# Kernel optimization log

Hardware: AMD Instinct MI355X
Metric: run time of the kernel (lower is better)

Reference implementation:

```python
import jax, jax.numpy as jnp
import numpy as np
from jax import lax


def conv2d(x, w, padding):
    # x: [B,C,H,W], w: [O,I,kh,kw]; torch Conv2d == cross-correlation, same as lax default
    return lax.conv_general_dilated(x, w, (1, 1), padding,
                                    dimension_numbers=('NCHW', 'OIHW', 'NCHW'))


def setup_inputs() -> dict:
    key = jax.random.key(0)
    ks = jax.random.split(key, 16)
    B, C1, C2, H1, W1, H2, W2, ratio = 8, 256, 512, 64, 64, 32, 32, 8
    Cr = C1 // ratio  # 32
    s = 0.05
    return {
        'x1': jax.random.normal(ks[0], (B, C1, H1, W1), jnp.float32),
        'x2': jax.random.normal(ks[1], (B, C2, H2, W2), jnp.float32),
        'wq': jax.random.normal(ks[2], (Cr, C1, 3, 3), jnp.float32) * s,
        'wk': jax.random.normal(ks[3], (Cr, C2, 3, 3), jnp.float32) * s,
        'wv': jax.random.normal(ks[4], (C1, C2, 3, 3), jnp.float32) * s,
        'wc': jax.random.normal(ks[5], (1, C1, 1, 1), jnp.float32) * s,
        'wch': jax.random.normal(ks[6], (C1, C1, 3, 3), jnp.float32) * s,
        'wt1': jax.random.normal(ks[7], (Cr, C1, 1, 1), jnp.float32) * s,
        'bt1': jax.random.normal(ks[8], (Cr,), jnp.float32) * s,
        'ln_g': jnp.ones((Cr, 1, 1), jnp.float32),
        'ln_b': jnp.zeros((Cr, 1, 1), jnp.float32),
        'wt2': jax.random.normal(ks[9], (C1, Cr, 1, 1), jnp.float32) * s,
        'bt2': jax.random.normal(ks[10], (C1,), jnp.float32) * s,
    }


def reference(x1, x2, wq, wk, wv, wc, wch, wt1, bt1, ln_g, ln_b, wt2, bt2):
    B, C1, H1, W1 = x1.shape
    N1 = H1 * W1
    N2 = x2.shape[2] * x2.shape[3]
    eps = 1e-5

    # spatial cross-attention branch
    q = conv2d(x1, wq, 'SAME').reshape(B, -1, N1)          # [B,Cr,N1]
    k = conv2d(x2, wk, 'SAME').reshape(B, -1, N2)          # [B,Cr,N2]
    v = conv2d(x2, wv, 'SAME').reshape(B, C1, N2)          # [B,C1,N2]
    content = jnp.einsum('bcn,bcm->bnm', k, q)             # [B,N2,N1] (key^T @ query)
    content = jax.nn.softmax(content, axis=1)              # softmax over N2 (dim=1)
    att_con = jnp.einsum('bcn,bnm->bcm', v, content).reshape(B, C1, H1, W1) + x1

    # channel attention branch
    cf = conv2d(x1, wc, 'VALID').reshape(B, 1, N1)         # 1x1 conv -> [B,1,N1]
    cf = jax.nn.softmax(cf.transpose(0, 2, 1), axis=1)     # [B,N1,1], softmax over N1
    chf = conv2d(x1, wch, 'SAME').reshape(B, C1, N1)       # [B,C1,N1]
    pool = jnp.einsum('bcn,bno->bco', chf, cf).reshape(B, C1, 1, 1)

    t = conv2d(pool, wt1, 'VALID') + bt1.reshape(1, -1, 1, 1)  # [B,Cr,1,1]
    mu = jnp.mean(t, axis=(1, 2, 3), keepdims=True)
    var = jnp.mean((t - mu) ** 2, axis=(1, 2, 3), keepdims=True)
    t = (t - mu) * lax.rsqrt(var + eps) * ln_g[None] + ln_b[None]
    t = jax.nn.relu(t)
    channel_weight = conv2d(t, wt2, 'VALID') + bt2.reshape(1, -1, 1, 1)  # [B,C1,1,1]

    return att_con + x1 * channel_weight
```

## Files before the change

kernel.cpp:

```cpp
#include <hip/hip_runtime.h>
#include <stdint.h>

#define LL long long

typedef short short8 __attribute__((ext_vector_type(8)));
typedef float f32x4 __attribute__((ext_vector_type(4)));
typedef unsigned int uint2v __attribute__((ext_vector_type(2)));

__device__ __forceinline__ unsigned short f2bf(float f) {
  unsigned u = __float_as_uint(f);
  unsigned r = (u + 0x7fffu + ((u >> 16) & 1u)) >> 16;
  return (unsigned short)r;
}
__device__ __forceinline__ float bf2f(unsigned short h) {
  return __uint_as_float(((unsigned)h) << 16);
}

#define MFMA16(A, B, C) __builtin_amdgcn_mfma_f32_16x16x32_bf16(A, B, C, 0, 0, 0)

__global__ __launch_bounds__(256) void wtrans2(
    const float* __restrict__ src, unsigned short* __restrict__ dh,
    unsigned short* __restrict__ dl, int OC, int IC)
{
  const int i = blockIdx.x * 256 + threadIdx.x;
  if (i >= OC * IC * 9) return;
  const int off = i % 9;
  const int rest = i / 9;
  const int ic = rest % IC;
  const int oc = rest / IC;
  const float v = src[i];
  const unsigned short h = f2bf(v);
  const LL di = (((LL)off * (IC >> 5) + (ic >> 5)) * OC + oc) * 32 + (ic & 31);
  dh[di] = h;
  if (dl) dl[di] = f2bf(v - bf2f(h));
}

__global__ __launch_bounds__(256) void transp(
    const float* __restrict__ src, unsigned short* __restrict__ dh,
    unsigned short* __restrict__ dl, int C, int N)
{
  __shared__ unsigned short sh[64 * 66];
  __shared__ unsigned short sl[64 * 66];
  const int t = threadIdx.x;
  const int b = blockIdx.z;
  const int n0 = blockIdx.x * 64, c0 = blockIdx.y * 64;
  {
    const int nl = t & 63, cl0 = t >> 6;
#pragma unroll
    for (int i = 0; i < 16; ++i) {
      const int cl = cl0 + 4 * i;
      const float v = src[((LL)b * C + c0 + cl) * N + n0 + nl];
      const unsigned short h = f2bf(v);
      sh[nl * 66 + cl] = h;
      sl[nl * 66 + cl] = f2bf(v - bf2f(h));
    }
  }
  __syncthreads();
  {
    const int cl = t & 63, nr0 = t >> 6;
    const int chunk = (c0 + cl) >> 5;
    const int cin = cl & 31;
#pragma unroll
    for (int j = 0; j < 16; ++j) {
      const int nr = nr0 + 4 * j;
      const LL di = (((LL)b * (C >> 5) + chunk) * N + n0 + nr) * 32 + cin;
      dh[di] = sh[nr * 66 + cl];
      if (dl) dl[di] = sl[nr * 66 + cl];
    }
  }
}

template<int NW>
__global__ __launch_bounds__(NW * 64) void conv_qk_s(
    const unsigned short* __restrict__ xh, const unsigned short* __restrict__ xl,
    const unsigned short* __restrict__ wh, const unsigned short* __restrict__ wl,
    unsigned short* __restrict__ dh, unsigned short* __restrict__ dl,
    int logW, int H)
{
  __shared__ float sred[NW][16][64];
  const int t = threadIdx.x, w = t >> 6, lane = t & 63;
  const int lo4 = lane & 15, hi4 = lane >> 4;
  const int b = blockIdx.z;
  const int W = 1 << logW;
  const int N = H * W;
  const int px0 = blockIdx.x * 32;
  const int row = px0 >> logW;
  const int x0 = px0 & (W - 1);
  const int ch = w;
  const short8 zero8 = {0, 0, 0, 0, 0, 0, 0, 0};

  f32x4 acc[2][2];
#pragma unroll
  for (int p = 0; p < 2; ++p)
#pragma unroll
    for (int ot = 0; ot < 2; ++ot) acc[p][ot] = (f32x4){0.f, 0.f, 0.f, 0.f};

  const LL xbase = ((LL)(b * NW + ch)) * N * 32 + hi4 * 8;
#pragma unroll
  for (int ky = 0; ky < 3; ++ky) {
    const int gy = row + ky - 1;
    const bool oky = (unsigned)gy < (unsigned)H;
    const int gyc = min(max(gy, 0), H - 1);
#pragma unroll
    for (int kx = 0; kx < 3; ++kx) {
      short8 Bh[2], Bl[2];
#pragma unroll
      for (int p = 0; p < 2; ++p) {
        const int gx = x0 + p * 16 + lo4 + kx - 1;
        const bool ok = oky && ((unsigned)gx < (unsigned)W);
        const int gxc = min(max(gx, 0), W - 1);
        const LL xoff = xbase + (LL)(gyc * W + gxc) * 32;
        const short8 bh = *(const short8*)(xh + xoff);
        const short8 bl = *(const short8*)(xl + xoff);
        Bh[p] = ok ? bh : zero8;
        Bl[p] = ok ? bl : zero8;
      }
      const int off = ky * 3 + kx;
      short8 Ah[2], Al[2];
#pragma unroll
      for (int ot = 0; ot < 2; ++ot) {
        const LL wi = ((LL)(off * NW + ch) * 32 + ot * 16 + lo4) * 32 + hi4 * 8;
        Ah[ot] = *(const short8*)(wh + wi);
        Al[ot] = *(const short8*)(wl + wi);
      }
#pragma unroll
      for (int p = 0; p < 2; ++p)
#pragma unroll
        for (int ot = 0; ot < 2; ++ot) {
          acc[p][ot] = MFMA16(Ah[ot], Bh[p], acc[p][ot]);
          acc[p][ot] = MFMA16(Ah[ot], Bl[p], acc[p][ot]);
          acc[p][ot] = MFMA16(Al[ot], Bh[p], acc[p][ot]);
        }
    }
  }
#pragma unroll
  for (int p = 0; p < 2; ++p)
#pragma unroll
    for (int ot = 0; ot < 2; ++ot)
#pragma unroll
      for (int r = 0; r < 4; ++r)
        sred[w][p * 8 + ot * 4 + r][lane] = acc[p][ot][r];
  __syncthreads();
  constexpr int SPW = 16 / NW;
#pragma unroll
  for (int si = 0; si < SPW; ++si) {
    const int slot = w * SPW + si;
    float v = sred[0][slot][lane];
#pragma unroll
    for (int j = 1; j < NW; ++j) v += sred[j][slot][lane];
    const int p = slot >> 3, ot = (slot >> 2) & 1, r = slot & 3;
    const LL di = ((LL)b * N + px0 + p * 16 + lo4) * 32 + ot * 16 + hi4 * 4 + r;
    const unsigned short h = f2bf(v);
    dh[di] = h;
    dl[di] = f2bf(v - bf2f(h));
  }
}

__global__ __launch_bounds__(512) void conv_v_s(
    const unsigned short* __restrict__ xh, const unsigned short* __restrict__ wt,
    unsigned short* __restrict__ out)
{
  __shared__ float sred[8][16][64];
  const int t = threadIdx.x, w = t >> 6, lane = t & 63;
  const int lo4 = lane & 15, hi4 = lane >> 4;
  const int b = blockIdx.z;
  const int tile = w & 1, kp = w >> 1;
  const int row = blockIdx.x * 2 + tile;
  const int ocb = blockIdx.y * 32;
  const short8 zero8 = {0, 0, 0, 0, 0, 0, 0, 0};

  f32x4 acc[2][2];
#pragma unroll
  for (int p = 0; p < 2; ++p)
#pragma unroll
    for (int o = 0; o < 2; ++o) acc[p][o] = (f32x4){0.f, 0.f, 0.f, 0.f};

  for (int ch = kp * 4; ch < kp * 4 + 4; ++ch) {
    const LL xchb = ((LL)(b * 16 + ch)) * 1024 * 32 + hi4 * 8;
#pragma unroll
    for (int ky = 0; ky < 3; ++ky) {
      const int gy = row + ky - 1;
      const bool oky = (unsigned)gy < 32u;
      const int gyc = min(max(gy, 0), 31);
#pragma unroll
      for (int kx = 0; kx < 3; ++kx) {
        short8 Bf[2];
#pragma unroll
        for (int p = 0; p < 2; ++p) {
          const int gx = p * 16 + lo4 + kx - 1;
          const bool ok = oky && ((unsigned)gx < 32u);
          const int gxc = min(max(gx, 0), 31);
          const short8 bv = *(const short8*)(xh + xchb + (LL)(gyc * 32 + gxc) * 32);
          Bf[p] = ok ? bv : zero8;
        }
        const int off = ky * 3 + kx;
        short8 Af[2];
#pragma unroll
        for (int o = 0; o < 2; ++o)
          Af[o] = *(const short8*)(
              wt + ((LL)(off * 16 + ch) * 256 + ocb + o * 16 + lo4) * 32 + hi4 * 8);
#pragma unroll
        for (int p = 0; p < 2; ++p)
#pragma unroll
          for (int o = 0; o < 2; ++o)
            acc[p][o] = MFMA16(Af[o], Bf[p], acc[p][o]);
      }
    }
  }
#pragma unroll
  for (int p = 0; p < 2; ++p)
#pragma unroll
    for (int o = 0; o < 2; ++o)
#pragma unroll
      for (int r = 0; r < 4; ++r)
        sred[w][p * 8 + o * 4 + r][lane] = acc[p][o][r];
  __syncthreads();
  const int tw = w & 1;
  const int rowt = blockIdx.x * 2 + tw;
#pragma unroll
  for (int si = 0; si < 4; ++si) {
    const int slot = (w >> 1) * 4 + si;
    const float v = sred[tw][slot][lane] + sred[2 + tw][slot][lane]
                  + sred[4 + tw][slot][lane] + sred[6 + tw][slot][lane];
    const int p = slot >> 3, o = (slot >> 2) & 1, r = slot & 3;
    const int oc = ocb + o * 16 + hi4 * 4 + r;
    out[(((LL)b * 32 + rowt) * 256 + oc) * 32 + p * 16 + lo4] = f2bf(v);
  }
}

__global__ __launch_bounds__(256) void cf_dot(
    const float* __restrict__ x1, const float* __restrict__ wc, float* __restrict__ cf)
{
  const int b = blockIdx.y;
  const int n = blockIdx.x * 256 + threadIdx.x;
  const float* xp = x1 + (LL)b * 256 * 4096 + n;
  float a = 0.f;
#pragma unroll 4
  for (int c = 0; c < 256; ++c)
    a = fmaf(xp[(LL)c * 4096], wc[c], a);
  cf[b * 4096 + n] = a;
}

__global__ __launch_bounds__(1024) void cf_softmax(
    const float* __restrict__ cf, float* __restrict__ cfs)
{
  const int b = blockIdx.x, t = threadIdx.x;
  __shared__ float r1[16];
  __shared__ float r2[16];
  float v[4];
#pragma unroll
  for (int j = 0; j < 4; ++j) v[j] = cf[b * 4096 + t + 1024 * j];
  float mx = fmaxf(fmaxf(v[0], v[1]), fmaxf(v[2], v[3]));
#pragma unroll
  for (int k = 1; k <= 32; k <<= 1) mx = fmaxf(mx, __shfl_xor(mx, k));
  const int wv = t >> 6;
  if ((t & 63) == 0) r1[wv] = mx;
  __syncthreads();
  float m2 = r1[0];
#pragma unroll
  for (int i = 1; i < 16; ++i) m2 = fmaxf(m2, r1[i]);
  float e[4]; float s = 0.f;
#pragma unroll
  for (int j = 0; j < 4; ++j) { e[j] = __expf(v[j] - m2); s += e[j]; }
#pragma unroll
  for (int k = 1; k <= 32; k <<= 1) s += __shfl_xor(s, k);
  if ((t & 63) == 0) r2[wv] = s;
  __syncthreads();
  float s2 = 0.f;
#pragma unroll
  for (int i = 0; i < 16; ++i) s2 += r2[i];
  const float inv = 1.f / s2;
#pragma unroll
  for (int j = 0; j < 4; ++j) cfs[b * 4096 + t + 1024 * j] = e[j] * inv;
}

__global__ __launch_bounds__(256) void ykern(
    const float* __restrict__ x1, const float* __restrict__ cfs, float* __restrict__ T)
{
  __shared__ float cl[6][64];
  const int chunk = blockIdx.x, b = blockIdx.y, t = threadIdx.x;
  for (int idx = t; idx < 384; idx += 256) {
    int lr = idx >> 6, col = idx & 63;
    int gr = chunk * 4 - 1 + lr;
    cl[lr][col] = ((unsigned)gr < 64u) ? cfs[b * 4096 + gr * 64 + col] : 0.f;
  }
  __syncthreads();
  const int c = t;
  float a[9];
#pragma unroll
  for (int k = 0; k < 9; ++k) a[k] = 0.f;
  const float* xp = x1 + ((LL)b * 256 + c) * 4096 + chunk * 256;
  for (int i = 0; i < 256; ++i) {
    float xv = xp[i];
    int yl = i >> 6, col = i & 63;
#pragma unroll
    for (int dy = 0; dy < 3; ++dy) {
      int lr = yl + 2 - dy;
#pragma unroll
      for (int dx = 0; dx < 3; ++dx) {
        int cc = col + 1 - dx;
        float f = ((unsigned)cc < 64u) ? cl[lr][cc] : 0.f;
        a[dy * 3 + dx] = fmaf(xv, f, a[dy * 3 + dx]);
      }
    }
  }
#pragma unroll
  for (int k = 0; k < 9; ++k)
    atomicAdd(&T[((LL)b * 256 + c) * 9 + k], a[k]);
}

__global__ __launch_bounds__(256) void pool_k(
    const float* __restrict__ T, const float* __restrict__ wch,
    float* __restrict__ pool)
{
  __shared__ __align__(16) float Tl[2304];
  const int b = blockIdx.y, ocg = blockIdx.x;
  const int t = threadIdx.x, w = t >> 6, lane = t & 63;
  for (int i = t; i < 2304; i += 256) Tl[i] = T[(LL)b * 2304 + i];
  __syncthreads();
  const float4* tp = (const float4*)Tl;
#pragma unroll
  for (int oi = 0; oi < 2; ++oi) {
    const int oc = ocg * 8 + w * 2 + oi;
    const float4* wp = (const float4*)(wch + (LL)oc * 2304);
    float a = 0.f;
#pragma unroll
    for (int j = 0; j < 9; ++j) {
      const int idx = lane + 64 * j;
      float4 w4 = wp[idx], t4 = tp[idx];
      a = fmaf(w4.x, t4.x, a); a = fmaf(w4.y, t4.y, a);
      a = fmaf(w4.z, t4.z, a); a = fmaf(w4.w, t4.w, a);
    }
#pragma unroll
    for (int k = 1; k <= 32; k <<= 1) a += __shfl_xor(a, k);
    if (lane == 0) pool[b * 256 + oc] = a;
  }
}

__global__ __launch_bounds__(256) void chw_tail(
    const float* __restrict__ pool_g,
    const float* __restrict__ wt1, const float* __restrict__ bt1,
    const float* __restrict__ lng, const float* __restrict__ lnb,
    const float* __restrict__ wt2, const float* __restrict__ bt2,
    float* __restrict__ cwp1)
{
  const int b = blockIdx.x, t = threadIdx.x;
  __shared__ float pool[256];
  __shared__ float tt[32];
  pool[t] = pool_g[b * 256 + t];
  __syncthreads();
  if (t < 64) {
    float tv = 0.f;
    if (t < 32) {
      const float* wp = wt1 + (LL)t * 256;
      for (int c = 0; c < 256; ++c) tv = fmaf(wp[c], pool[c], tv);
      tv += bt1[t];
    }
    float s = tv;
#pragma unroll
    for (int k = 1; k <= 16; k <<= 1) s += __shfl_xor(s, k);
    float mu = s * (1.f / 32.f);
    float d = tv - mu;
    float vs = d * d;
#pragma unroll
    for (int k = 1; k <= 16; k <<= 1) vs += __shfl_xor(vs, k);
    float var = vs * (1.f / 32.f);
    if (t < 32) {
      float nrm = d / sqrtf(var + 1e-5f);
      float y = nrm * lng[t] + lnb[t];
      tt[t] = fmaxf(y, 0.f);
    }
  }
  __syncthreads();
  {
    float s2 = bt2[t];
    const float* wp = wt2 + (LL)t * 32;
#pragma unroll
    for (int i = 0; i < 32; ++i) s2 = fmaf(wp[i], tt[i], s2);
    cwp1[b * 256 + t] = 1.f + s2;
  }
}

__global__ __launch_bounds__(256) void attn_stats(
    const unsigned short* __restrict__ qh_g, const unsigned short* __restrict__ ql_g,
    const unsigned short* __restrict__ kh_g, const unsigned short* __restrict__ kl_g,
    float* __restrict__ mxs, float* __restrict__ invl)
{
  const int t = threadIdx.x, w = t >> 6, lane = t & 63;
  const int lo4 = lane & 15, hi4 = lane >> 4;
  const int b = blockIdx.y, mc = blockIdx.x * 64;
  const float L2E = 1.4426950408889634f;

  short8 qh[4], ql[4];
#pragma unroll
  for (int mt = 0; mt < 4; ++mt) {
    const LL qa = ((LL)(b * 4096 + mc + mt * 16 + lo4)) * 32 + hi4 * 8;
    qh[mt] = *(const short8*)(qh_g + qa);
    ql[mt] = *(const short8*)(ql_g + qa);
  }

  float M[4], L[4];
#pragma unroll
  for (int mt = 0; mt < 4; ++mt) { M[mt] = -1e30f; L[mt] = 0.f; }

  for (int ns = 0; ns < 16; ++ns) {
    const int n = w * 256 + ns * 16 + lo4;
    const LL ka = ((LL)(b * 1024 + n)) * 32 + hi4 * 8;
    const short8 kh = *(const short8*)(kh_g + ka);
    const short8 kl = *(const short8*)(kl_g + ka);
#pragma unroll
    for (int mt = 0; mt < 4; ++mt) {
      f32x4 s = {0.f, 0.f, 0.f, 0.f};
      s = MFMA16(kl, qh[mt], s);
      s = MFMA16(kh, ql[mt], s);
      s = MFMA16(kh, qh[mt], s);
      float lm = fmaxf(fmaxf(s[0], s[1]), fmaxf(s[2], s[3]));
      float nM = fmaxf(M[mt], lm);
      float sc = exp2f((M[mt] - nM) * L2E);
      L[mt] = L[mt] * sc + exp2f((s[0] - nM) * L2E) + exp2f((s[1] - nM) * L2E)
                         + exp2f((s[2] - nM) * L2E) + exp2f((s[3] - nM) * L2E);
      M[mt] = nM;
    }
  }
#pragma unroll
  for (int mask = 16; mask <= 32; mask <<= 1) {
#pragma unroll
    for (int mt = 0; mt < 4; ++mt) {
      float oM = __shfl_xor(M[mt], mask), oL = __shfl_xor(L[mt], mask);
      float nM = fmaxf(M[mt], oM);
      L[mt] = L[mt] * exp2f((M[mt] - nM) * L2E) + oL * exp2f((oM - nM) * L2E);
      M[mt] = nM;
    }
  }
  __shared__ float sM[4][64], sL[4][64];
  if (lane < 16) {
#pragma unroll
    for (int mt = 0; mt < 4; ++mt) {
      sM[w][mt * 16 + lane] = M[mt];
      sL[w][mt * 16 + lane] = L[mt];
    }
  }
  __syncthreads();
  if (t < 64) {
    float Mg = sM[0][t], Lg = sL[0][t];
#pragma unroll
    for (int wv = 1; wv < 4; ++wv) {
      float oM = sM[wv][t], oL = sL[wv][t];
      float nM = fmaxf(Mg, oM);
      Lg = Lg * exp2f((Mg - nM) * L2E) + oL * exp2f((oM - nM) * L2E);
      Mg = nM;
    }
    mxs[b * 4096 + mc + t] = Mg * L2E;
    invl[b * 4096 + mc + t] = 1.f / Lg;
  }
}

__global__ __launch_bounds__(256) void attn_pv(
    const unsigned short* __restrict__ qh_g, const unsigned short* __restrict__ ql_g,
    const unsigned short* __restrict__ kh_g, const unsigned short* __restrict__ kl_g,
    const unsigned short* __restrict__ v16,
    const float* __restrict__ mxs, const float* __restrict__ invl,
    const float* __restrict__ x1, const float* __restrict__ cwp1,
    float* __restrict__ out)
{
  __shared__ __align__(16) unsigned short Pt[2][32][136];
  const int t = threadIdx.x, w = t >> 6, lane = t & 63;
  const int lo4 = lane & 15, hi4 = lane >> 4;
  const int b = blockIdx.y, mb = blockIdx.x * 32;
  const float L2E = 1.4426950408889634f;

  short8 qh[2], ql[2];
  float mxv[2], ilv[2];
#pragma unroll
  for (int mt = 0; mt < 2; ++mt) {
    const int m = mb + mt * 16 + lo4;
    const LL qa = ((LL)(b * 4096 + m)) * 32 + hi4 * 8;
    qh[mt] = *(const short8*)(qh_g + qa);
    ql[mt] = *(const short8*)(ql_g + qa);
    mxv[mt] = mxs[b * 4096 + m];
    ilv[mt] = invl[b * 4096 + m];
  }

  f32x4 acc[4][2];
#pragma unroll
  for (int ct = 0; ct < 4; ++ct)
#pragma unroll
    for (int mt = 0; mt < 2; ++mt) acc[ct][mt] = (f32x4){0.f, 0.f, 0.f, 0.f};

  short8 kh[2], kl[2];
#pragma unroll
  for (int ns = 0; ns < 2; ++ns) {
    const LL ka = ((LL)(b * 1024 + w * 32 + ns * 16 + lo4)) * 32 + hi4 * 8;
    kh[ns] = *(const short8*)(kh_g + ka);
    kl[ns] = *(const short8*)(kl_g + ka);
  }

  int buf = 0;
  for (int nt = 0; nt < 8; ++nt) {
    short8 knh[2], knl[2];
    {
      const int ntn = (nt + 1) & 7;
#pragma unroll
      for (int ns = 0; ns < 2; ++ns) {
        const LL ka = ((LL)(b * 1024 + ntn * 128 + w * 32 + ns * 16 + lo4)) * 32 + hi4 * 8;
        knh[ns] = *(const short8*)(kh_g + ka);
        knl[ns] = *(const short8*)(kl_g + ka);
      }
    }
    f32x4 s[2][2];
#pragma unroll
    for (int ns = 0; ns < 2; ++ns)
#pragma unroll
      for (int mt = 0; mt < 2; ++mt) {
        f32x4 z = {0.f, 0.f, 0.f, 0.f};
        z = MFMA16(kl[ns], qh[mt], z);
        z = MFMA16(kh[ns], ql[mt], z);
        z = MFMA16(kh[ns], qh[mt], z);
        s[ns][mt] = z;
      }
    short8 vpre[2][4];
#pragma unroll
    for (int ks = 0; ks < 2; ++ks)
#pragma unroll
      for (int ct = 0; ct < 4; ++ct)
        vpre[ks][ct] = *(const short8*)(
            v16 + (((LL)b * 32 + nt * 4 + ks) * 256 + w * 64 + ct * 16 + lo4) * 32 + hi4 * 8);
#pragma unroll
    for (int ns = 0; ns < 2; ++ns)
#pragma unroll
      for (int mt = 0; mt < 2; ++mt) {
        const int m_loc = mt * 16 + lo4;
        const int nl = w * 32 + ns * 16 + hi4 * 4;
        float p0 = exp2f(fmaf(s[ns][mt][0], L2E, -mxv[mt])) * ilv[mt];
        float p1 = exp2f(fmaf(s[ns][mt][1], L2E, -mxv[mt])) * ilv[mt];
        float p2 = exp2f(fmaf(s[ns][mt][2], L2E, -mxv[mt])) * ilv[mt];
        float p3 = exp2f(fmaf(s[ns][mt][3], L2E, -mxv[mt])) * ilv[mt];
        uint2v u;
        u[0] = (unsigned)f2bf(p0) | ((unsigned)f2bf(p1) << 16);
        u[1] = (unsigned)f2bf(p2) | ((unsigned)f2bf(p3) << 16);
        *(uint2v*)&Pt[buf][m_loc][nl] = u;
      }
    __syncthreads();
#pragma unroll
    for (int ks = 0; ks < 4; ++ks) {
      short8 pb[2];
#pragma unroll
      for (int mt = 0; mt < 2; ++mt)
        pb[mt] = *(const short8*)&Pt[buf][mt * 16 + lo4][ks * 32 + hi4 * 8];
#pragma unroll
      for (int ct = 0; ct < 4; ++ct) {
        const short8 va = (ks < 2)
            ? vpre[ks][ct]
            : *(const short8*)(
                  v16 + (((LL)b * 32 + nt * 4 + ks) * 256 + w * 64 + ct * 16 + lo4) * 32 + hi4 * 8);
#pragma unroll
        for (int mt = 0; mt < 2; ++mt)
          acc[ct][mt] = MFMA16(va, pb[mt], acc[ct][mt]);
      }
    }
    buf ^= 1;
#pragma unroll
    for (int ns = 0; ns < 2; ++ns) { kh[ns] = knh[ns]; kl[ns] = knl[ns]; }
  }

#pragma unroll
  for (int ct = 0; ct < 4; ++ct)
#pragma unroll
    for (int mt = 0; mt < 2; ++mt) {
      const int m = mb + mt * 16 + lo4;
#pragma unroll
      for (int r = 0; r < 4; ++r) {
        const int c = w * 64 + ct * 16 + hi4 * 4 + r;
        const float cw = cwp1[b * 256 + c];
        const LL off = ((LL)(b * 256 + c)) * 4096 + m;
        out[off] = acc[ct][mt][r] + x1[off] * cw;
      }
    }
}

extern "C" void kernel_launch(void* const* d_in, const int* in_sizes, int n_in,
                              void* d_out, int out_size, void* d_ws, size_t ws_size,
                              hipStream_t stream) {
  const float* x1  = (const float*)d_in[0];
  const float* x2  = (const float*)d_in[1];
  const float* wq  = (const float*)d_in[2];
  const float* wk  = (const float*)d_in[3];
  const float* wv  = (const float*)d_in[4];
  const float* wc  = (const float*)d_in[5];
  const float* wch = (const float*)d_in[6];
  const float* wt1 = (const float*)d_in[7];
  const float* bt1 = (const float*)d_in[8];
  const float* lng = (const float*)d_in[9];
  const float* lnb = (const float*)d_in[10];
  const float* wt2 = (const float*)d_in[11];
  const float* bt2 = (const float*)d_in[12];
  float* outp = (float*)d_out;

  float* ws   = (float*)d_ws;
  float* qtf  = ws;
  float* ktf  = qtf + 1048576;
  float* mxsb = ktf + 262144;
  float* invb = mxsb + 32768;
  float* cfr  = invb + 32768;
  float* cfs  = cfr + 32768;
  float* Tb   = cfs + 32768;
  float* cwb  = Tb + 18432;
  unsigned short* sbase = (unsigned short*)(cwb + 2048);
  unsigned short* v16  = sbase;
  unsigned short* x1th = v16  + 2097152;
  unsigned short* x1tl = x1th + 8388608;
  unsigned short* x2th = x1tl + 8388608;
  unsigned short* x2tl = x2th + 4194304;
  unsigned short* wvt  = x2tl + 4194304;
  unsigned short* wqh  = wvt  + 1179648;
  unsigned short* wql  = wqh  + 73728;
  unsigned short* wkh  = wql  + 73728;
  unsigned short* wkl  = wkh  + 147456;

  unsigned short* qhg = (unsigned short*)qtf;
  unsigned short* qlg = qhg + 1048576;
  unsigned short* khg = (unsigned short*)ktf;
  unsigned short* klg = khg + 262144;

  hipMemsetAsync(Tb, 0, (size_t)18432 * 4, stream);

  wtrans2<<<dim3(4608), 256, 0, stream>>>(wv, wvt, nullptr, 256, 512);
  wtrans2<<<dim3(288),  256, 0, stream>>>(wq, wqh, wql, 32, 256);
  wtrans2<<<dim3(576),  256, 0, stream>>>(wk, wkh, wkl, 32, 512);

  transp<<<dim3(64, 4, 8), 256, 0, stream>>>(x1, x1th, x1tl, 256, 4096);
  transp<<<dim3(16, 8, 8), 256, 0, stream>>>(x2, x2th, x2tl, 512, 1024);

  conv_qk_s<16><<<dim3(32, 1, 8), 1024, 0, stream>>>(
      x2th, x2tl, wkh, wkl, khg, klg, 5, 32);

  conv_v_s<<<dim3(16, 8, 8), 512, 0, stream>>>(x2th, wvt, v16);

  conv_qk_s<8><<<dim3(128, 1, 8), 512, 0, stream>>>(
      x1th, x1tl, wqh, wql, qhg, qlg, 6, 64);

  cf_dot<<<dim3(16, 8), 256, 0, stream>>>(x1, wc, cfr);
  cf_softmax<<<dim3(8), 1024, 0, stream>>>(cfr, cfs);
  ykern<<<dim3(16, 8), 256, 0, stream>>>(x1, cfs, Tb);
  pool_k<<<dim3(32, 8), 256, 0, stream>>>(Tb, wch, cfr);
  chw_tail<<<dim3(8), 256, 0, stream>>>(cfr, wt1, bt1, lng, lnb, wt2, bt2, cwb);

  attn_stats<<<dim3(64, 8), 256, 0, stream>>>(qhg, qlg, khg, klg, mxsb, invb);
  attn_pv<<<dim3(128, 8), 256, 0, stream>>>(qhg, qlg, khg, klg, v16, mxsb, invb, x1, cwb, outp);
}
```

Measured before the change: 427.7 us.

## Restructure V conv to reuse weight fragments across four output rows

```diff
diff --git a/kernel.cpp b/kernel.cpp
--- a/kernel.cpp
+++ b/kernel.cpp
@@ -156,75 +156,87 @@
   }
 }
 
-__global__ __launch_bounds__(512) void conv_v_s(
+__global__ __launch_bounds__(512) void conv_v_w(
     const unsigned short* __restrict__ xh, const unsigned short* __restrict__ wt,
     unsigned short* __restrict__ out)
 {
-  __shared__ float sred[8][16][64];
+  __shared__ float sred[4][32][64];
   const int t = threadIdx.x, w = t >> 6, lane = t & 63;
   const int lo4 = lane & 15, hi4 = lane >> 4;
   const int b = blockIdx.z;
-  const int tile = w & 1, kp = w >> 1;
-  const int row = blockIdx.x * 2 + tile;
-  const int ocb = blockIdx.y * 32;
+  const int h = w & 1, ocg = (w >> 1) & 1, kp = w >> 2;
+  const int r0 = blockIdx.x * 4;
+  const int ocb = blockIdx.y * 64 + ocg * 32;
   const short8 zero8 = {0, 0, 0, 0, 0, 0, 0, 0};
 
-  f32x4 acc[2][2];
-#pragma unroll
-  for (int p = 0; p < 2; ++p)
-#pragma unroll
-    for (int o = 0; o < 2; ++o) acc[p][o] = (f32x4){0.f, 0.f, 0.f, 0.f};
-
-  for (int ch = kp * 4; ch < kp * 4 + 4; ++ch) {
+  f32x4 acc[4][2];
+#pragma unroll
+  for (int rr = 0; rr < 4; ++rr)
+#pragma unroll
+    for (int ot = 0; ot < 2; ++ot) acc[rr][ot] = (f32x4){0.f, 0.f, 0.f, 0.f};
+
+  for (int ch = kp * 8; ch < kp * 8 + 8; ++ch) {
+    short8 A[3][3][2];
+#pragma unroll
+    for (int ky = 0; ky < 3; ++ky)
+#pragma unroll
+      for (int kx = 0; kx < 3; ++kx)
+#pragma unroll
+        for (int ot = 0; ot < 2; ++ot) {
+          const int off = ky * 3 + kx;
+          A[ky][kx][ot] = *(const short8*)(
+              wt + ((LL)(off * 16 + ch) * 256 + ocb + ot * 16 + lo4) * 32 + hi4 * 8);
+        }
     const LL xchb = ((LL)(b * 16 + ch)) * 1024 * 32 + hi4 * 8;
 #pragma unroll
-    for (int ky = 0; ky < 3; ++ky) {
-      const int gy = row + ky - 1;
+    for (int g = 0; g < 6; ++g) {
+      const int gy = r0 - 1 + g;
       const bool oky = (unsigned)gy < 32u;
       const int gyc = min(max(gy, 0), 31);
+      short8 Bg[3];
 #pragma unroll
       for (int kx = 0; kx < 3; ++kx) {
-        short8 Bf[2];
-#pragma unroll
-        for (int p = 0; p < 2; ++p) {
-          const int gx = p * 16 + lo4 + kx - 1;
-          const bool ok = oky && ((unsigned)gx < 32u);
-          const int gxc = min(max(gx, 0), 31);
-          const short8 bv = *(const short8*)(xh + xchb + (LL)(gyc * 32 + gxc) * 32);
-          Bf[p] = ok ? bv : zero8;
+        const int gx = h * 16 + lo4 + kx - 1;
+        const bool ok = oky && ((unsigned)gx < 32u);
+        const int gxc = min(max(gx, 0), 31);
+        const short8 bv = *(const short8*)(xh + xchb + (LL)(gyc * 32 + gxc) * 32);
+        Bg[kx] = ok ? bv : zero8;
+      }
+#pragma unroll
+      for (int rr = 0; rr < 4; ++rr) {
+        if (rr > g || rr + 2 < g) continue;
+        const int ky = g - rr;
+#pragma unroll
+        for (int kx = 0; kx < 3; ++kx)
+#pragma unroll
+          for (int ot = 0; ot < 2; ++ot)
+            acc[rr][ot] = MFMA16(A[ky][kx][ot], Bg[kx], acc[rr][ot]);
+      }
+    }
+  }
+  const int slotbase = h * 2 + ocg;
+  if (kp == 1) {
+#pragma unroll
+    for (int rr = 0; rr < 4; ++rr)
+#pragma unroll
+      for (int ot = 0; ot < 2; ++ot)
+#pragma unroll
+        for (int r = 0; r < 4; ++r)
+          sred[slotbase][rr * 8 + ot * 4 + r][lane] = acc[rr][ot][r];
+  }
+  __syncthreads();
+  if (kp == 0) {
+#pragma unroll
+    for (int rr = 0; rr < 4; ++rr)
+#pragma unroll
+      for (int ot = 0; ot < 2; ++ot)
+#pragma unroll
+        for (int r = 0; r < 4; ++r) {
+          const float v = acc[rr][ot][r] + sred[slotbase][rr * 8 + ot * 4 + r][lane];
+          const int row = r0 + rr;
+          const int oc = ocb + ot * 16 + hi4 * 4 + r;
+          out[(((LL)b * 32 + row) * 256 + oc) * 32 + h * 16 + lo4] = f2bf(v);
         }
-        const int off = ky * 3 + kx;
-        short8 Af[2];
-#pragma unroll
-        for (int o = 0; o < 2; ++o)
-          Af[o] = *(const short8*)(
-              wt + ((LL)(off * 16 + ch) * 256 + ocb + o * 16 + lo4) * 32 + hi4 * 8);
-#pragma unroll
-        for (int p = 0; p < 2; ++p)
-#pragma unroll
-          for (int o = 0; o < 2; ++o)
-            acc[p][o] = MFMA16(Af[o], Bf[p], acc[p][o]);
-      }
-    }
-  }
-#pragma unroll
-  for (int p = 0; p < 2; ++p)
-#pragma unroll
-    for (int o = 0; o < 2; ++o)
-#pragma unroll
-      for (int r = 0; r < 4; ++r)
-        sred[w][p * 8 + o * 4 + r][lane] = acc[p][o][r];
-  __syncthreads();
-  const int tw = w & 1;
-  const int rowt = blockIdx.x * 2 + tw;
-#pragma unroll
-  for (int si = 0; si < 4; ++si) {
-    const int slot = (w >> 1) * 4 + si;
-    const float v = sred[tw][slot][lane] + sred[2 + tw][slot][lane]
-                  + sred[4 + tw][slot][lane] + sred[6 + tw][slot][lane];
-    const int p = slot >> 3, o = (slot >> 2) & 1, r = slot & 3;
-    const int oc = ocb + o * 16 + hi4 * 4 + r;
-    out[(((LL)b * 32 + rowt) * 256 + oc) * 32 + p * 16 + lo4] = f2bf(v);
   }
 }
 
@@ -634,7 +646,7 @@
   conv_qk_s<16><<<dim3(32, 1, 8), 1024, 0, stream>>>(
       x2th, x2tl, wkh, wkl, khg, klg, 5, 32);
 
-  conv_v_s<<<dim3(16, 8, 8), 512, 0, stream>>>(x2th, wvt, v16);
+  conv_v_w<<<dim3(8, 4, 8), 512, 0, stream>>>(x2th, wvt, v16);
 
   conv_qk_s<8><<<dim3(128, 1, 8), 512, 0, stream>>>(
       x1th, x1tl, wqh, wql, qhg, qlg, 6, 64);
```

Result: faster. 417.9 us (-2.3%).
